# Kernel tuning notes

Measured on AMD Instinct MI355X. Metric: run time of the kernel, lower is better.

## Reference

```python
import jax, jax.numpy as jnp
import numpy as np
from jax import lax

B, C, H, W = 32, 64, 56, 56
G = 4            # num_heads*2 with num_heads=2
SMK, K = 5, 7
C2 = C // 2
HEAD_DIM = C // G
SCALE = HEAD_DIM ** -0.5


def _bias_idx(k, h, w):
    # static replica of ContMix.generate_idx + apply_rpb index construction
    rpb_size = 2 * k - 1
    idx_h = np.arange(k)
    idx_w = np.arange(k)
    idx_k = (idx_h[:, None] * rpb_size + idx_w).reshape(-1)
    rep_h = np.ones(k, np.int64); rep_h[k // 2] = h - (k - 1)
    rep_w = np.ones(k, np.int64); rep_w[k // 2] = w - (k - 1)
    bias_hw = np.repeat(idx_h, rep_h)[:, None] * rpb_size + np.repeat(idx_w, rep_w)  # (h, w)
    bias_idx = (bias_hw[..., None] + idx_k).reshape(-1, k * k)[::-1]  # torch.flip dim 0
    return jnp.asarray(bias_idx.copy())

IDX1 = _bias_idx(SMK, H, W)
IDX2 = _bias_idx(K, H, W)


def setup_inputs() -> dict:
    key = jax.random.key(0)
    ks = jax.random.split(key, 18)
    r = lambda i, sh: jax.random.normal(ks[i], sh, jnp.float32)
    return dict(
        x=r(0, (B, C, H, W)),
        lepe_w=r(1, (C, 1, K, K)) * 0.1,
        lepe_b=r(2, (C,)) * 0.1,
        lepe_bn_s=1.0 + 0.1 * r(3, (C,)),
        lepe_bn_b=0.1 * r(4, (C,)),
        wq_w=r(5, (C2, C2)) * (C2 ** -0.5),
        wq_bn_s=1.0 + 0.1 * r(6, (C2,)),
        wq_bn_b=0.1 * r(7, (C2,)),
        wk_w=r(8, (C2, C2)) * (C2 ** -0.5),
        wk_bn_s=1.0 + 0.1 * r(9, (C2,)),
        wk_bn_b=0.1 * r(10, (C2,)),
        wp_w=r(11, (SMK * SMK + K * K, 49)) * (49 ** -0.5),
        wp_b=0.1 * r(12, (SMK * SMK + K * K,)),
        rpb1=0.02 * r(13, (G, 2 * SMK - 1, 2 * SMK - 1)),
        rpb2=0.02 * r(14, (G, 2 * K - 1, 2 * K - 1)),
        dy_w=r(15, (C, C)) * (C ** -0.5),
        dy_bn_s=1.0 + 0.1 * r(16, (C,)),
        dy_bn_b=0.1 * r(17, (C,)),
    )


def _per_ch(t):
    return t[None, :, None, None]


def _contmix(x, lepe_w, lepe_b, lepe_bn_s, lepe_bn_b, wq_w, wq_bn_s, wq_bn_b,
             wk_w, wk_bn_s, wk_bn_b, wp_w, wp_b, rpb1, rpb2, dy_w, dy_bn_s, dy_bn_b):
    # lepe: deploy-mode DilatedReparamBlock = depthwise 7x7 conv (+bias), then eval BN
    lepe = lax.conv_general_dilated(x, lepe_w, (1, 1), [(K // 2, K // 2)] * 2,
                                    feature_group_count=C)
    lepe = (lepe + _per_ch(lepe_b)) * _per_ch(lepe_bn_s) + _per_ch(lepe_bn_b)

    q, kf = jnp.split(x, 2, axis=1)                         # (B, C2, H, W) each
    q = jnp.einsum('oi,bihw->bohw', wq_w, q)                # weight_query 1x1 conv
    q = (q * _per_ch(wq_bn_s) + _per_ch(wq_bn_b)) * SCALE
    # weight_key: AdaptiveAvgPool2d(7) -> 1x1 conv -> BN (H,W divisible by 7)
    kp = kf.reshape(B, C2, 7, H // 7, 7, W // 7).mean(axis=(3, 5))
    kp = jnp.einsum('oi,bihw->bohw', wk_w, kp)
    kp = kp * _per_ch(wk_bn_s) + _per_ch(wk_bn_b)

    qg = q.reshape(B, G, C2 // G, H * W)                    # b g c n
    kg = kp.reshape(B, G, C2 // G, 49)                      # b g c l
    w = jnp.einsum('bgcn,bgcl->bgnl', qg, kg)               # (B, G, HW, 49)
    # weight_proj: 1x1 conv over the 49 pooled-context channels
    w = jnp.einsum('ml,bgnl->bgnm', wp_w, w) + wp_b         # (B, G, HW, 74)
    w = w.reshape(B, G, H, W, SMK * SMK + K * K)

    attn1 = w[..., :SMK * SMK]
    attn2 = w[..., SMK * SMK:]
    attn1 = attn1 + rpb1.reshape(G, -1)[:, IDX1].reshape(1, G, H, W, SMK * SMK)
    attn2 = attn2 + rpb2.reshape(G, -1)[:, IDX2].reshape(1, G, H, W, K * K)
    attn1 = jax.nn.softmax(attn1, axis=-1)
    attn2 = jax.nn.softmax(attn2, axis=-1)

    c = C // (2 * G)                                        # value head dim = 8
    v = x.reshape(B, 2, G, c, H, W)                         # 'b (m g c) h w'

    def dyn_mix(attn, val, k):
        # unfold + einsum: content-adaptive depthwise mixing
        p = lax.conv_general_dilated_patches(
            val.reshape(B, G * c, H, W), (k, k), (1, 1), [(k // 2, k // 2)] * 2,
            dimension_numbers=('NCHW', 'OIHW', 'NCHW'))
        p = p.reshape(B, G, c, k * k, H, W)                 # channel-major patch layout
        return jnp.einsum('bgckhw,bghwk->bgchw', p, attn)

    x1 = dyn_mix(attn1, v[:, 0], SMK)
    x2 = dyn_mix(attn2, v[:, 1], K)
    out = jnp.concatenate([x1, x2], axis=1).reshape(B, C, H, W)
    out = jnp.einsum('oi,bihw->bohw', dy_w, out)            # dyconv_proj 1x1 + BN
    out = out * _per_ch(dy_bn_s) + _per_ch(dy_bn_b)
    return out + lepe


def reference(x, lepe_w, lepe_b, lepe_bn_s, lepe_bn_b, wq_w, wq_bn_s, wq_bn_b,
              wk_w, wk_bn_s, wk_bn_b, wp_w, wp_b, rpb1, rpb2, dy_w, dy_bn_s, dy_bn_b):
    return _contmix(x, lepe_w, lepe_b, lepe_bn_s, lepe_bn_b, wq_w, wq_bn_s, wq_bn_b,
                    wk_w, wk_bn_s, wk_bn_b, wp_w, wp_b, rpb1, rpb2, dy_w, dy_bn_s, dy_bn_b)
```

## Files before the change

### kernel.cpp

```cpp
#include <hip/hip_runtime.h>

#define BB 32
#define CC 64
#define C2 32
#define HH 56
#define WW 56
#define HW 3136

__global__ __launch_bounds__(256) void lepe_k(const float* __restrict__ x,
                                              const float* __restrict__ wt,
                                              const float* __restrict__ b,
                                              const float* __restrict__ s,
                                              const float* __restrict__ bb,
                                              float* __restrict__ out) {
    const int bc = blockIdx.y;
    const int c = bc & 63;
    const int qi = blockIdx.x * 256 + threadIdx.x;
    if (qi >= 784) return;
    const int r = qi / 14;
    const int c4 = (qi % 14) * 4;
    const float* wp = wt + c * 49;
    const float* xp = x + (long)bc * HW;
    float acc0 = 0.f, acc1 = 0.f, acc2 = 0.f, acc3 = 0.f;
    #pragma unroll
    for (int i = 0; i < 7; ++i) {
        const int y = r + i - 3;
        if ((unsigned)y >= HH) continue;
        const float4* row = reinterpret_cast<const float4*>(xp + y * WW + c4 - 4);
        float4 A = make_float4(0.f, 0.f, 0.f, 0.f);
        float4 Cv = make_float4(0.f, 0.f, 0.f, 0.f);
        if (c4 != 0) A = row[0];
        const float4 Bv = row[1];
        if (c4 != 52) Cv = row[2];
        const float w12[12] = {A.x, A.y, A.z, A.w, Bv.x, Bv.y, Bv.z, Bv.w, Cv.x, Cv.y, Cv.z, Cv.w};
        #pragma unroll
        for (int j = 0; j < 7; ++j) {
            const float wv = wp[i * 7 + j];
            acc0 = fmaf(w12[j + 1], wv, acc0);
            acc1 = fmaf(w12[j + 2], wv, acc1);
            acc2 = fmaf(w12[j + 3], wv, acc2);
            acc3 = fmaf(w12[j + 4], wv, acc3);
        }
    }
    const float bc_ = b[c], sc = s[c], bbc = bb[c];
    float4 res;
    res.x = (acc0 + bc_) * sc + bbc;
    res.y = (acc1 + bc_) * sc + bbc;
    res.z = (acc2 + bc_) * sc + bbc;
    res.w = (acc3 + bc_) * sc + bbc;
    *reinterpret_cast<float4*>(out + (long)bc * HW + r * WW + c4) = res;
}

__global__ __launch_bounds__(256) void prep_k(const float* __restrict__ x,
                                              const float* __restrict__ wk,
                                              const float* __restrict__ wks,
                                              const float* __restrict__ wkb,
                                              const float* __restrict__ wp_w,
                                              float* __restrict__ WK) {
    __shared__ float p_s[32 * 49];
    __shared__ float kg_s[8 * 49];
    const int b = blockIdx.x >> 2;
    const int g = blockIdx.x & 3;
    const int tid = threadIdx.x;
    for (int idx = tid; idx < 1568; idx += 256) {
        const int i = idx / 49, l = idx % 49;
        const int py = l / 7, px = l % 7;
        const float4* xp4 = reinterpret_cast<const float4*>(
            x + ((long)(b * CC + 32 + i)) * HW + py * 8 * WW + px * 8);
        float4 sA = make_float4(0.f, 0.f, 0.f, 0.f);
        float4 sB = make_float4(0.f, 0.f, 0.f, 0.f);
        #pragma unroll
        for (int y = 0; y < 8; ++y) {
            const float4 a = xp4[y * 14];
            const float4 c = xp4[y * 14 + 1];
            sA.x += a.x; sA.y += a.y; sA.z += a.z; sA.w += a.w;
            sB.x += c.x; sB.y += c.y; sB.z += c.z; sB.w += c.w;
        }
        p_s[idx] = (sA.x + sA.y + sA.z + sA.w + sB.x + sB.y + sB.z + sB.w) * (1.f / 64.f);
    }
    __syncthreads();
    for (int idx = tid; idx < 392; idx += 256) {
        const int o8 = idx / 49, l = idx % 49;
        const int o = g * 8 + o8;
        float acc = 0.f;
        #pragma unroll
        for (int i = 0; i < 32; ++i) acc = fmaf(wk[o * 32 + i], p_s[i * 49 + l], acc);
        kg_s[idx] = acc * wks[o] + wkb[o];
    }
    __syncthreads();
    for (int idx = tid; idx < 640; idx += 256) {
        const int c = idx / 80, slot = idx % 80;
        float acc = 0.f;
        int m = -1;
        if (slot < 28) { if (slot < 25) m = slot; }
        else           { if (slot < 77) m = 25 + (slot - 28); }
        if (m >= 0) {
            const float* kp = kg_s + c * 49;
            #pragma unroll
            for (int l = 0; l < 49; ++l) acc = fmaf(wp_w[m * 49 + l], kp[l], acc);
        }
        const long base = (long)blockIdx.x * 640;
        if (slot < 28) WK[base + c * 28 + slot] = acc;
        else           WK[base + 224 + c * 52 + (slot - 28)] = acc;
    }
}

__global__ __launch_bounds__(256) void attnmix_k(const float* __restrict__ x,
                                                 const float* __restrict__ WK,
                                                 const float* __restrict__ wq_w,
                                                 const float* __restrict__ wq_s,
                                                 const float* __restrict__ wq_bb,
                                                 const float* __restrict__ wp_b,
                                                 const float* __restrict__ rpb1,
                                                 const float* __restrict__ rpb2,
                                                 float* __restrict__ mix) {
    __shared__ float WK1_s[8 * 28];
    __shared__ float WK2_s[8 * 52];
    __shared__ float wqT_s[32 * 8];
    __shared__ float wpb1_s[25];
    __shared__ float wpb2_s[49];
    __shared__ float rpb1_s[81];
    __shared__ float rpb2_s[169];
    __shared__ float wqbn_s[16];
    const int tid = threadIdx.x;
    const int bg = blockIdx.y;
    const int g = bg & 3, b = bg >> 2;
    {
        const float* wkp = WK + (long)bg * 640;
        for (int i = tid; i < 224; i += 256) WK1_s[i] = wkp[i];
        for (int i = tid; i < 416; i += 256) WK2_s[i] = wkp[224 + i];
    }
    if (tid < 256) {
        const int i = tid >> 3, c = tid & 7;
        wqT_s[tid] = wq_w[(g * 8 + c) * 32 + i];
    }
    if (tid < 25) wpb1_s[tid] = wp_b[tid];
    if (tid >= 32 && tid < 81) wpb2_s[tid - 32] = wp_b[25 + tid - 32];
    if (tid < 81) rpb1_s[tid] = rpb1[g * 81 + tid];
    if (tid < 169) rpb2_s[tid] = rpb2[g * 169 + tid];
    if (tid >= 192 && tid < 200) wqbn_s[tid - 192] = wq_s[g * 8 + tid - 192];
    if (tid >= 200 && tid < 208) wqbn_s[8 + tid - 200] = wq_bb[g * 8 + tid - 200];
    __syncthreads();
    const int n = blockIdx.x * 256 + tid;
    if (n >= HW) return;

    const int ph = n / WW, pw = n % WW;
    const int yr = HH - 1 - ph, xr = WW - 1 - pw;

    const float* xb = x + (long)b * CC * HW + n;

    float q8[8];
    #pragma unroll
    for (int c = 0; c < 8; ++c) q8[c] = 0.f;
    for (int i = 0; i < 32; ++i) {
        const float xv = xb[i * HW];
        #pragma unroll
        for (int c = 0; c < 8; ++c) q8[c] = fmaf(wqT_s[i * 8 + c], xv, q8[c]);
    }
    #pragma unroll
    for (int c = 0; c < 8; ++c)
        q8[c] = (q8[c] * wqbn_s[c] + wqbn_s[8 + c]) * 0.25f;

    __builtin_amdgcn_sched_barrier(0);

    {
        float w1[25];
        #pragma unroll
        for (int m = 0; m < 25; ++m) w1[m] = wpb1_s[m];
        #pragma unroll
        for (int c = 0; c < 8; ++c) {
            const float qv = q8[c];
            #pragma unroll
            for (int m = 0; m < 25; ++m) w1[m] = fmaf(qv, WK1_s[c * 28 + m], w1[m]);
        }
        const int rh5 = yr < 2 ? yr : (yr > 53 ? yr - 51 : 2);
        const int rw5 = xr < 2 ? xr : (xr > 53 ? xr - 51 : 2);
        #pragma unroll
        for (int i = 0; i < 5; ++i)
            #pragma unroll
            for (int j = 0; j < 5; ++j)
                w1[i * 5 + j] += rpb1_s[(rh5 + i) * 9 + (rw5 + j)];
        float mx = -1e30f;
        #pragma unroll
        for (int m = 0; m < 25; ++m) mx = fmaxf(mx, w1[m]);
        float sm = 0.f;
        #pragma unroll
        for (int m = 0; m < 25; ++m) { w1[m] = __expf(w1[m] - mx); sm += w1[m]; }
        const float r = 1.f / sm;
        #pragma unroll
        for (int m = 0; m < 25; ++m) w1[m] *= r;

        const float* vb = xb + (long)(g * 8) * HW;
        float acc[8];
        #pragma unroll
        for (int ch = 0; ch < 8; ++ch) acc[ch] = 0.f;
        #pragma unroll
        for (int i = 0; i < 5; ++i) {
            const int y = ph + i - 2;
            if ((unsigned)y >= HH) continue;
            #pragma unroll
            for (int j = 0; j < 5; ++j) {
                const int xx = pw + j - 2;
                if ((unsigned)xx >= WW) continue;
                const int off = (i - 2) * WW + (j - 2);
                const float wv = w1[i * 5 + j];
                #pragma unroll
                for (int ch = 0; ch < 8; ++ch)
                    acc[ch] = fmaf(wv, vb[ch * HW + off], acc[ch]);
            }
        }
        float* m0 = mix + ((long)b * CC + g * 8) * HW + n;
        #pragma unroll
        for (int ch = 0; ch < 8; ++ch) m0[ch * HW] = acc[ch];
    }

    __builtin_amdgcn_sched_barrier(0);

    {
        float w2[49];
        #pragma unroll
        for (int m = 0; m < 49; ++m) w2[m] = wpb2_s[m];
        #pragma unroll
        for (int c = 0; c < 8; ++c) {
            const float qv = q8[c];
            #pragma unroll
            for (int m = 0; m < 49; ++m) w2[m] = fmaf(qv, WK2_s[c * 52 + m], w2[m]);
        }
        const int rh7 = yr < 3 ? yr : (yr > 52 ? yr - 49 : 3);
        const int rw7 = xr < 3 ? xr : (xr > 52 ? xr - 49 : 3);
        #pragma unroll
        for (int i = 0; i < 7; ++i)
            #pragma unroll
            for (int j = 0; j < 7; ++j)
                w2[i * 7 + j] += rpb2_s[(rh7 + i) * 13 + (rw7 + j)];
        float mx = -1e30f;
        #pragma unroll
        for (int m = 0; m < 49; ++m) mx = fmaxf(mx, w2[m]);
        float sm = 0.f;
        #pragma unroll
        for (int m = 0; m < 49; ++m) { w2[m] = __expf(w2[m] - mx); sm += w2[m]; }
        const float r = 1.f / sm;
        #pragma unroll
        for (int m = 0; m < 49; ++m) w2[m] *= r;

        const float* vb = xb + (long)(32 + g * 8) * HW;
        float acc[8];
        #pragma unroll
        for (int ch = 0; ch < 8; ++ch) acc[ch] = 0.f;
        #pragma unroll
        for (int i = 0; i < 7; ++i) {
            const int y = ph + i - 3;
            if ((unsigned)y >= HH) continue;
            #pragma unroll
            for (int j = 0; j < 7; ++j) {
                const int xx = pw + j - 3;
                if ((unsigned)xx >= WW) continue;
                const int off = (i - 3) * WW + (j - 3);
                const float wv = w2[i * 7 + j];
                #pragma unroll
                for (int ch = 0; ch < 8; ++ch)
                    acc[ch] = fmaf(wv, vb[ch * HW + off], acc[ch]);
            }
        }
        float* m1 = mix + ((long)b * CC + 32 + g * 8) * HW + n;
        #pragma unroll
        for (int ch = 0; ch < 8; ++ch) m1[ch * HW] = acc[ch];
    }
}

__global__ __launch_bounds__(256) void final_k(const float* __restrict__ mix,
                                               const float* __restrict__ dy_w,
                                               const float* __restrict__ s,
                                               const float* __restrict__ bb,
                                               float* __restrict__ out) {
    __shared__ float w_s[64 * 64];
    const int tid = threadIdx.x;
    const int b = blockIdx.y;
    for (int i = tid; i < 4096; i += 256) w_s[(i & 63) * 64 + (i >> 6)] = dy_w[i];
    __syncthreads();
    const int oo = (tid >> 5) * 8;
    const int p4 = blockIdx.x * 32 + (tid & 31);
    if (p4 >= 784) return;
    const float* mp = mix + (long)b * CC * HW + p4 * 4;
    float4 acc[8];
    #pragma unroll
    for (int o = 0; o < 8; ++o) acc[o] = make_float4(0.f, 0.f, 0.f, 0.f);
    for (int i = 0; i < 64; ++i) {
        const float4 mv = *reinterpret_cast<const float4*>(mp + (long)i * HW);
        const float* wr = w_s + i * 64 + oo;
        #pragma unroll
        for (int o = 0; o < 8; ++o) {
            const float wv = wr[o];
            acc[o].x = fmaf(wv, mv.x, acc[o].x);
            acc[o].y = fmaf(wv, mv.y, acc[o].y);
            acc[o].z = fmaf(wv, mv.z, acc[o].z);
            acc[o].w = fmaf(wv, mv.w, acc[o].w);
        }
    }
    float* op = out + (long)b * CC * HW + p4 * 4;
    #pragma unroll
    for (int o = 0; o < 8; ++o) {
        const float sc = s[oo + o], bc = bb[oo + o];
        float4* dst = reinterpret_cast<float4*>(op + (long)(oo + o) * HW);
        float4 prev = *dst;
        prev.x = fmaf(acc[o].x, sc, bc) + prev.x;
        prev.y = fmaf(acc[o].y, sc, bc) + prev.y;
        prev.z = fmaf(acc[o].z, sc, bc) + prev.z;
        prev.w = fmaf(acc[o].w, sc, bc) + prev.w;
        *dst = prev;
    }
}

extern "C" void kernel_launch(void* const* d_in, const int* in_sizes, int n_in,
                              void* d_out, int out_size, void* d_ws, size_t ws_size,
                              hipStream_t stream) {
    const float* x       = (const float*)d_in[0];
    const float* lepe_w  = (const float*)d_in[1];
    const float* lepe_b  = (const float*)d_in[2];
    const float* lepe_s  = (const float*)d_in[3];
    const float* lepe_bb = (const float*)d_in[4];
    const float* wq_w    = (const float*)d_in[5];
    const float* wq_s    = (const float*)d_in[6];
    const float* wq_bb   = (const float*)d_in[7];
    const float* wk_w    = (const float*)d_in[8];
    const float* wk_s    = (const float*)d_in[9];
    const float* wk_bb   = (const float*)d_in[10];
    const float* wp_w    = (const float*)d_in[11];
    const float* wp_b    = (const float*)d_in[12];
    const float* rpb1    = (const float*)d_in[13];
    const float* rpb2    = (const float*)d_in[14];
    const float* dy_w    = (const float*)d_in[15];
    const float* dy_s    = (const float*)d_in[16];
    const float* dy_bb   = (const float*)d_in[17];
    float* out = (float*)d_out;

    float* ws     = (float*)d_ws;
    float* WK_ws  = ws;
    float* mix_ws = WK_ws + 128 * 640;

    const int nTiles = (HW + 255) / 256;

    lepe_k<<<dim3(4, BB * CC), 256, 0, stream>>>(x, lepe_w, lepe_b, lepe_s, lepe_bb, out);
    prep_k<<<dim3(BB * 4), 256, 0, stream>>>(x, wk_w, wk_s, wk_bb, wp_w, WK_ws);
    attnmix_k<<<dim3(nTiles, BB * 4), 256, 0, stream>>>(x, WK_ws, wq_w, wq_s, wq_bb,
                                                        wp_b, rpb1, rpb2, mix_ws);
    final_k<<<dim3(25, BB), 256, 0, stream>>>(mix_ws, dy_w, dy_s, dy_bb, out);
}
```

Before: 249.8 us.

## Fuse depthwise lepe conv into attnmix kernel with shared-memory halo tiles

Removes the separate lepe depthwise 7x7 kernel and computes it inside attnmix_k, reusing the value channels that are already being read. Each block stages an 8-channel halo tile (12 rows x 64 cols) of the value channels into LDS, once for the 5x5 branch and once for the 7x7 branch, and both the dynamic mix and the lepe conv read from that tile instead of strided global loads. This is meant to drop one full read of x and a kernel launch, and to turn the many redundant global gathers into LDS reads. In exchange it adds extra LDS traffic and syncs, raises LDS use (about 25KB per block), which may reduce occupancy, and the lepe output is written before final_k, which must then accumulate onto it.

```diff
diff --git a/kernel.cpp b/kernel.cpp
--- a/kernel.cpp
+++ b/kernel.cpp
@@ -2,54 +2,11 @@
 
 #define BB 32
 #define CC 64
-#define C2 32
 #define HH 56
 #define WW 56
 #define HW 3136
-
-__global__ __launch_bounds__(256) void lepe_k(const float* __restrict__ x,
-                                              const float* __restrict__ wt,
-                                              const float* __restrict__ b,
-                                              const float* __restrict__ s,
-                                              const float* __restrict__ bb,
-                                              float* __restrict__ out) {
-    const int bc = blockIdx.y;
-    const int c = bc & 63;
-    const int qi = blockIdx.x * 256 + threadIdx.x;
-    if (qi >= 784) return;
-    const int r = qi / 14;
-    const int c4 = (qi % 14) * 4;
-    const float* wp = wt + c * 49;
-    const float* xp = x + (long)bc * HW;
-    float acc0 = 0.f, acc1 = 0.f, acc2 = 0.f, acc3 = 0.f;
-    #pragma unroll
-    for (int i = 0; i < 7; ++i) {
-        const int y = r + i - 3;
-        if ((unsigned)y >= HH) continue;
-        const float4* row = reinterpret_cast<const float4*>(xp + y * WW + c4 - 4);
-        float4 A = make_float4(0.f, 0.f, 0.f, 0.f);
-        float4 Cv = make_float4(0.f, 0.f, 0.f, 0.f);
-        if (c4 != 0) A = row[0];
-        const float4 Bv = row[1];
-        if (c4 != 52) Cv = row[2];
-        const float w12[12] = {A.x, A.y, A.z, A.w, Bv.x, Bv.y, Bv.z, Bv.w, Cv.x, Cv.y, Cv.z, Cv.w};
-        #pragma unroll
-        for (int j = 0; j < 7; ++j) {
-            const float wv = wp[i * 7 + j];
-            acc0 = fmaf(w12[j + 1], wv, acc0);
-            acc1 = fmaf(w12[j + 2], wv, acc1);
-            acc2 = fmaf(w12[j + 3], wv, acc2);
-            acc3 = fmaf(w12[j + 4], wv, acc3);
-        }
-    }
-    const float bc_ = b[c], sc = s[c], bbc = bb[c];
-    float4 res;
-    res.x = (acc0 + bc_) * sc + bbc;
-    res.y = (acc1 + bc_) * sc + bbc;
-    res.z = (acc2 + bc_) * sc + bbc;
-    res.w = (acc3 + bc_) * sc + bbc;
-    *reinterpret_cast<float4*>(out + (long)bc * HW + r * WW + c4) = res;
-}
+#define TW 64
+#define TR 12
 
 __global__ __launch_bounds__(256) void prep_k(const float* __restrict__ x,
                                               const float* __restrict__ wk,
@@ -113,7 +70,13 @@
                                                  const float* __restrict__ wp_b,
                                                  const float* __restrict__ rpb1,
                                                  const float* __restrict__ rpb2,
-                                                 float* __restrict__ mix) {
+                                                 const float* __restrict__ lw,
+                                                 const float* __restrict__ lb,
+                                                 const float* __restrict__ ls,
+                                                 const float* __restrict__ lbb,
+                                                 float* __restrict__ mix,
+                                                 float* __restrict__ out) {
+    __shared__ float tile[8 * TR * TW];
     __shared__ float WK1_s[8 * 28];
     __shared__ float WK2_s[8 * 52];
     __shared__ float wqT_s[32 * 8];
@@ -122,15 +85,18 @@
     __shared__ float rpb1_s[81];
     __shared__ float rpb2_s[169];
     __shared__ float wqbn_s[16];
+    __shared__ float lw_s[16 * 49];
+    __shared__ float lbn_s[48];
     const int tid = threadIdx.x;
     const int bg = blockIdx.y;
     const int g = bg & 3, b = bg >> 2;
+
     {
         const float* wkp = WK + (long)bg * 640;
         for (int i = tid; i < 224; i += 256) WK1_s[i] = wkp[i];
         for (int i = tid; i < 416; i += 256) WK2_s[i] = wkp[224 + i];
     }
-    if (tid < 256) {
+    {
         const int i = tid >> 3, c = tid & 7;
         wqT_s[tid] = wq_w[(g * 8 + c) * 32 + i];
     }
@@ -140,14 +106,43 @@
     if (tid < 169) rpb2_s[tid] = rpb2[g * 169 + tid];
     if (tid >= 192 && tid < 200) wqbn_s[tid - 192] = wq_s[g * 8 + tid - 192];
     if (tid >= 200 && tid < 208) wqbn_s[8 + tid - 200] = wq_bb[g * 8 + tid - 200];
-    __syncthreads();
-    const int n = blockIdx.x * 256 + tid;
-    if (n >= HW) return;
-
-    const int ph = n / WW, pw = n % WW;
+    for (int i = tid; i < 784; i += 256) {
+        const int ch = i / 49, k = i % 49;
+        const int c = (ch < 8) ? (g * 8 + ch) : (32 + g * 8 + ch - 8);
+        lw_s[i] = lw[c * 49 + k];
+    }
+    if (tid < 16) {
+        const int c = (tid < 8) ? (g * 8 + tid) : (32 + g * 8 + tid - 8);
+        lbn_s[tid] = lb[c]; lbn_s[16 + tid] = ls[c]; lbn_s[32 + tid] = lbb[c];
+    }
+
+    const int N0 = blockIdx.x << 8;
+    const int ph0 = N0 / WW;
+    const int r0 = ph0 - 3;
+
+    {
+        const float* xc = x + ((long)b * CC + g * 8) * HW;
+        #pragma unroll
+        for (int ch = 0; ch < 8; ++ch)
+            for (int k = tid; k < TR * TW; k += 256) {
+                const int row = k >> 6, lxx = k & 63;
+                const int gy = r0 + row, gx = lxx - 3;
+                float v = 0.f;
+                if ((unsigned)gy < HH && (unsigned)gx < WW) v = xc[ch * HW + gy * WW + gx];
+                tile[ch * (TR * TW) + k] = v;
+            }
+    }
+    __syncthreads();
+
+    const int n = N0 + tid;
+    const bool valid = n < HW;
+    const int nc = valid ? n : HW - 1;
+    const int ph = nc / WW, pw = nc % WW;
     const int yr = HH - 1 - ph, xr = WW - 1 - pw;
-
-    const float* xb = x + (long)b * CC * HW + n;
+    const int lrow = ph - r0;
+    const int tb0 = (lrow - 3) * TW + pw;
+
+    const float* xb = x + (long)b * CC * HW + nc;
 
     float q8[8];
     #pragma unroll
@@ -190,31 +185,43 @@
         #pragma unroll
         for (int m = 0; m < 25; ++m) w1[m] *= r;
 
-        const float* vb = xb + (long)(g * 8) * HW;
-        float acc[8];
-        #pragma unroll
-        for (int ch = 0; ch < 8; ++ch) acc[ch] = 0.f;
-        #pragma unroll
-        for (int i = 0; i < 5; ++i) {
-            const int y = ph + i - 2;
-            if ((unsigned)y >= HH) continue;
-            #pragma unroll
-            for (int j = 0; j < 5; ++j) {
-                const int xx = pw + j - 2;
-                if ((unsigned)xx >= WW) continue;
-                const int off = (i - 2) * WW + (j - 2);
-                const float wv = w1[i * 5 + j];
+        float* m0 = mix + ((long)b * CC + g * 8) * HW + nc;
+        float* o0 = out + ((long)b * CC + g * 8) * HW + nc;
+        #pragma unroll
+        for (int ch = 0; ch < 8; ++ch) {
+            const float* t = tile + ch * (TR * TW) + tb0;
+            const float* lwc = lw_s + ch * 49;
+            float a = 0.f, la = 0.f;
+            #pragma unroll
+            for (int i = 0; i < 7; ++i)
                 #pragma unroll
-                for (int ch = 0; ch < 8; ++ch)
-                    acc[ch] = fmaf(wv, vb[ch * HW + off], acc[ch]);
+                for (int j = 0; j < 7; ++j) {
+                    const float v = t[i * TW + j];
+                    la = fmaf(lwc[i * 7 + j], v, la);
+                    if (i >= 1 && i <= 5 && j >= 1 && j <= 5)
+                        a = fmaf(w1[(i - 1) * 5 + (j - 1)], v, a);
+                }
+            if (valid) {
+                m0[ch * HW] = a;
+                o0[ch * HW] = (la + lbn_s[ch]) * lbn_s[16 + ch] + lbn_s[32 + ch];
             }
         }
-        float* m0 = mix + ((long)b * CC + g * 8) * HW + n;
-        #pragma unroll
-        for (int ch = 0; ch < 8; ++ch) m0[ch * HW] = acc[ch];
-    }
-
-    __builtin_amdgcn_sched_barrier(0);
+    }
+
+    __syncthreads();
+    {
+        const float* xc = x + ((long)b * CC + 32 + g * 8) * HW;
+        #pragma unroll
+        for (int ch = 0; ch < 8; ++ch)
+            for (int k = tid; k < TR * TW; k += 256) {
+                const int row = k >> 6, lxx = k & 63;
+                const int gy = r0 + row, gx = lxx - 3;
+                float v = 0.f;
+                if ((unsigned)gy < HH && (unsigned)gx < WW) v = xc[ch * HW + gy * WW + gx];
+                tile[ch * (TR * TW) + k] = v;
+            }
+    }
+    __syncthreads();
 
     {
         float w2[49];
@@ -243,28 +250,26 @@
         #pragma unroll
         for (int m = 0; m < 49; ++m) w2[m] *= r;
 
-        const float* vb = xb + (long)(32 + g * 8) * HW;
-        float acc[8];
-        #pragma unroll
-        for (int ch = 0; ch < 8; ++ch) acc[ch] = 0.f;
-        #pragma unroll
-        for (int i = 0; i < 7; ++i) {
-            const int y = ph + i - 3;
-            if ((unsigned)y >= HH) continue;
-            #pragma unroll
-            for (int j = 0; j < 7; ++j) {
-                const int xx = pw + j - 3;
-                if ((unsigned)xx >= WW) continue;
-                const int off = (i - 3) * WW + (j - 3);
-                const float wv = w2[i * 7 + j];
+        float* m1 = mix + ((long)b * CC + 32 + g * 8) * HW + nc;
+        float* o1 = out + ((long)b * CC + 32 + g * 8) * HW + nc;
+        #pragma unroll
+        for (int ch = 0; ch < 8; ++ch) {
+            const float* t = tile + ch * (TR * TW) + tb0;
+            const float* lwc = lw_s + (8 + ch) * 49;
+            float a = 0.f, la = 0.f;
+            #pragma unroll
+            for (int i = 0; i < 7; ++i)
                 #pragma unroll
-                for (int ch = 0; ch < 8; ++ch)
-                    acc[ch] = fmaf(wv, vb[ch * HW + off], acc[ch]);
+                for (int j = 0; j < 7; ++j) {
+                    const float v = t[i * TW + j];
+                    la = fmaf(lwc[i * 7 + j], v, la);
+                    a = fmaf(w2[i * 7 + j], v, a);
+                }
+            if (valid) {
+                m1[ch * HW] = a;
+                o1[ch * HW] = (la + lbn_s[8 + ch]) * lbn_s[16 + 8 + ch] + lbn_s[32 + 8 + ch];
             }
         }
-        float* m1 = mix + ((long)b * CC + 32 + g * 8) * HW + n;
-        #pragma unroll
-        for (int ch = 0; ch < 8; ++ch) m1[ch * HW] = acc[ch];
     }
 }
 
@@ -340,9 +345,10 @@
 
     const int nTiles = (HW + 255) / 256;
 
-    lepe_k<<<dim3(4, BB * CC), 256, 0, stream>>>(x, lepe_w, lepe_b, lepe_s, lepe_bb, out);
     prep_k<<<dim3(BB * 4), 256, 0, stream>>>(x, wk_w, wk_s, wk_bb, wp_w, WK_ws);
     attnmix_k<<<dim3(nTiles, BB * 4), 256, 0, stream>>>(x, WK_ws, wq_w, wq_s, wq_bb,
-                                                        wp_b, rpb1, rpb2, mix_ws);
+                                                        wp_b, rpb1, rpb2,
+                                                        lepe_w, lepe_b, lepe_s, lepe_bb,
+                                                        mix_ws, out);
     final_k<<<dim3(25, BB), 256, 0, stream>>>(mix_ws, dy_w, dy_s, dy_bb, out);
 }
```

New measurement: 243.5 us. -2.5%, faster.
